# Kernel optimization log

Measured on AMD Instinct MI355X. Metric: run time of the kernel, lower is better.

## Reference

```python
import jax, jax.numpy as jnp
import numpy as np
import math

B, S, D = 4, 2048, 1024
NUM_HEADS = 16
HEAD_DIM = D // NUM_HEADS


def setup_inputs() -> dict:
    key = jax.random.key(0)
    ks = jax.random.split(key, 6)
    scale = 1.0 / math.sqrt(D)
    batch = jax.random.normal(ks[0], (B, S, D), dtype=jnp.float32)
    w_query = jax.random.normal(ks[1], (D, D), dtype=jnp.float32) * scale
    w_key = jax.random.normal(ks[2], (D, D), dtype=jnp.float32) * scale
    w_value = jax.random.normal(ks[3], (D, D), dtype=jnp.float32) * scale
    out_w = jax.random.normal(ks[4], (D, D), dtype=jnp.float32) * scale
    out_b = jax.random.normal(ks[5], (D,), dtype=jnp.float32) * 0.01
    return {"batch": batch, "w_query": w_query, "w_key": w_key,
            "w_value": w_value, "out_w": out_w, "out_b": out_b}


def reference(batch, w_query, w_key, w_value, out_w, out_b):
    b, s, _ = batch.shape
    # QKV projections (Linear with no bias): x @ W^T, here weights stored as [D,D] applied as x@W
    q = (batch @ w_query).reshape(b, s, NUM_HEADS, HEAD_DIM)
    k = (batch @ w_key).reshape(b, s, NUM_HEADS, HEAD_DIM)
    v = (batch @ w_value).reshape(b, s, NUM_HEADS, HEAD_DIM)
    # scores: [b, h, s, s]
    scores = jnp.einsum('bqhd,bkhd->bhqk', q, k)
    causal = jnp.tril(jnp.ones((s, s), dtype=bool))
    scores = jnp.where(causal, scores, -jnp.inf)
    # original divides by sqrt(head_dim) AFTER masking (-inf stays -inf)
    weights = jax.nn.softmax(scores / math.sqrt(HEAD_DIM), axis=-1)
    # dropout_percent = 0 -> identity
    out = jnp.einsum('bhqk,bkhd->bqhd', weights, v).reshape(b, s, D)
    return out @ out_w + out_b
```

## Files before the change

### kernel.cpp

```cpp
#include <hip/hip_runtime.h>
#include <hip/hip_bf16.h>

#define S_LEN 2048
#define D_DIM 1024
#define NHEAD 16
#define HDIM  64
#define BATCH 4
#define MROWS (BATCH*S_LEN)
#define QKV_LD 3072

typedef short bf16x8 __attribute__((ext_vector_type(8)));
typedef float f32x4  __attribute__((ext_vector_type(4)));
typedef float f32x16 __attribute__((ext_vector_type(16)));
typedef unsigned short u16;

#if __has_builtin(__builtin_amdgcn_exp2f)
#define EXP2(x) __builtin_amdgcn_exp2f(x)
#else
#define EXP2(x) __expf((x) * 0.6931471805599453f)
#endif

__device__ inline u16 f2bf(float f) {
  union { float f; unsigned u; } v; v.f = f;
  unsigned r = v.u + 0x7fff + ((v.u >> 16) & 1);
  return (u16)(r >> 16);
}

__device__ inline unsigned cvtpk(float lo, float hi_) {
  unsigned d;
  asm("v_cvt_pk_bf16_f32 %0, %1, %2" : "=v"(d) : "v"(lo), "v"(hi_));
  return d;
}

__device__ inline void perm32swap(unsigned& a, unsigned& b) {
  asm volatile("v_permlane32_swap_b32 %0, %1" : "+v"(a), "+v"(b));
}

__device__ inline void gload_lds16(const void* g, void* l) {
  __builtin_amdgcn_global_load_lds(
      (const __attribute__((address_space(1))) void*)g,
      (__attribute__((address_space(3))) void*)l, 16, 0, 0);
}

__global__ void cvt_x_kernel(const float* __restrict__ x, u16* __restrict__ xb, int n4) {
  int i = blockIdx.x * 256 + threadIdx.x;
  if (i >= n4) return;
  float4 v = reinterpret_cast<const float4*>(x)[i];
  ushort4 o;
  o.x = f2bf(v.x); o.y = f2bf(v.y); o.z = f2bf(v.z); o.w = f2bf(v.w);
  reinterpret_cast<ushort4*>(xb)[i] = o;
}

__global__ void transpose_w_kernel(const float* __restrict__ w, u16* __restrict__ wt) {
  __shared__ float t[32][33];
  int tx = threadIdx.x, ty = threadIdx.y;
  int n0 = blockIdx.x * 32, k0 = blockIdx.y * 32;
#pragma unroll
  for (int j = 0; j < 32; j += 8)
    t[ty + j][tx] = w[(size_t)(k0 + ty + j) * D_DIM + n0 + tx];
  __syncthreads();
#pragma unroll
  for (int j = 0; j < 32; j += 8)
    wt[(size_t)(n0 + ty + j) * D_DIM + k0 + tx] = f2bf(t[tx][ty + j]);
}

__global__ __launch_bounds__(256) void pack_k_kernel(const u16* __restrict__ QKV,
                                                     u16* __restrict__ KP) {
  int tid = threadIdx.x;
  int j = blockIdx.x, bh = blockIdx.y;
  int s = tid >> 6, lane = tid & 63;
  int lq = lane & 31, hi = lane >> 5;
  int b = bh >> 4, h = bh & 15;
  const u16* src = QKV + (size_t)(b * S_LEN + j * 32 + lq) * QKV_LD
                   + 1024 + h * HDIM + s * 16 + hi * 8;
  bf16x8 v = *(const bf16x8*)src;
  *(bf16x8*)(KP + ((size_t)(bh * 64 + j) * 4 + s) * 512 + lane * 8) = v;
}

__global__ __launch_bounds__(256) void pack_v_kernel(const u16* __restrict__ QKV,
                                                     u16* __restrict__ VP) {
  int tid = threadIdx.x;
  int j = blockIdx.x, bh = blockIdx.y;
  int c = tid >> 6, lane = tid & 63;
  int lq = lane & 31, hi = lane >> 5;
  int b = bh >> 4, h = bh & 15;
  int d = (c >> 1) * 32 + lq;
  int s0 = j * 32 + (c & 1) * 16 + hi * 8;
  const u16* src = QKV + (size_t)(b * S_LEN + s0) * QKV_LD + 2048 + h * HDIM + d;
  u16 tmp[8];
#pragma unroll
  for (int e = 0; e < 8; ++e) tmp[e] = src[(size_t)e * QKV_LD];
  *(bf16x8*)(VP + ((size_t)(bh * 64 + j) * 4 + c) * 512 + lane * 8) = *(bf16x8*)tmp;
}

#define BAR() asm volatile("s_barrier" ::: "memory")
#define WAITV(N) asm volatile("s_waitcnt vmcnt(" #N ")" ::: "memory")
#define PRIO1() __builtin_amdgcn_s_setprio(1)
#define PRIO0() __builtin_amdgcn_s_setprio(0)

#define STAGE(bufv, ab, h, gptr) {                                              \
  const u16* _s = (gptr) + (size_t)(wid * 8 + (lane >> 3)) * 1024               \
                  + (size_t)((((lane & 7) ^ (lane >> 3)) * 8));                 \
  gload_lds16(_s,              &lds[bufv][ab][(h) * 8192 + wid * 512]);         \
  gload_lds16(_s + 64 * 1024,  &lds[bufv][ab][(h) * 8192 + 4096 + wid * 512]); }

#define RDF(bufv, ab, r_, c2_) \
  (*(const bf16x8*)((const char*)&lds[bufv][ab][0] + ((r_) * 128 + ((c2_) ^ rxA))))

#define READ_ALO(bufv) { _Pragma("unroll") for (int mt = 0; mt < 4; mt++)       \
  _Pragma("unroll") for (int ks = 0; ks < 2; ks++)                              \
    fa[mt][ks] = RDF(bufv, 0, wm + mt * 16 + fr, ks * 64 + fq * 16); }
#define READ_AHI(bufv) { _Pragma("unroll") for (int mt = 0; mt < 4; mt++)       \
  _Pragma("unroll") for (int ks = 0; ks < 2; ks++)                              \
    fa[4 + mt][ks] = RDF(bufv, 0, wm + 64 + mt * 16 + fr, ks * 64 + fq * 16); }
#define READ_BLO(bufv) { _Pragma("unroll") for (int nt = 0; nt < 2; nt++)       \
  _Pragma("unroll") for (int ks = 0; ks < 2; ks++)                              \
    fb[nt][ks] = RDF(bufv, 1, wn + nt * 16 + fr, ks * 64 + fq * 16); }
#define READ_BHI(bufv) { _Pragma("unroll") for (int nt = 0; nt < 2; nt++)       \
  _Pragma("unroll") for (int ks = 0; ks < 2; ks++)                              \
    fb[2 + nt][ks] = RDF(bufv, 1, wn + 32 + nt * 16 + fr, ks * 64 + fq * 16); }

#define QUAD(mh, nh) { PRIO1();                                                 \
  _Pragma("unroll") for (int mt = 0; mt < 4; mt++)                              \
  _Pragma("unroll") for (int nt = 0; nt < 2; nt++)                              \
  _Pragma("unroll") for (int ks = 0; ks < 2; ks++)                              \
    acc[(mh) * 4 + mt][(nh) * 2 + nt] = __builtin_amdgcn_mfma_f32_16x16x32_bf16(\
        fa[(mh) * 4 + mt][ks], fb[(nh) * 2 + nt][ks],                           \
        acc[(mh) * 4 + mt][(nh) * 2 + nt], 0, 0, 0);                            \
  PRIO0(); }

#define APTR(h, kt) (A  + (size_t)(bm * 256 + (h) * 128) * 1024 + (size_t)(kt) * 64)
#define BPTR(h, kt) (Bt + (size_t)(bn * 256 + (h) * 128) * 1024 + (size_t)(kt) * 64)

template <int EPI>
__global__ __launch_bounds__(512, 2) void gemm8p_kernel(
    const u16* __restrict__ A, const u16* __restrict__ Bt,
    void* __restrict__ Cv, const float* __restrict__ bias, int nbx, int ldc) {
  __shared__ u16 lds[2][2][16384];
  const int tid = threadIdx.x, wid = tid >> 6, lane = tid & 63;
  const int fr = lane & 15, fq = lane >> 4;
  const int wm = (wid >> 2) * 128, wn = (wid & 3) * 64;
  const int rxA = (fr & 7) << 4;
  const int nwg = gridDim.x, cpx = nwg >> 3, wg = blockIdx.x;
  const int swz = (wg & 7) * cpx + (wg >> 3);
  const int bm = swz / nbx, bn = swz % nbx;

  bf16x8 fa[8][2], fb[4][2];
  f32x4 acc[8][4] = {};

  STAGE(0, 0, 0, APTR(0, 0)); STAGE(0, 0, 1, APTR(1, 0));
  STAGE(0, 1, 0, BPTR(0, 0)); STAGE(0, 1, 1, BPTR(1, 0));
  STAGE(1, 0, 0, APTR(0, 1)); STAGE(1, 0, 1, APTR(1, 1));
  WAITV(4);
  BAR();

  for (int i = 0; i < 8; i++) {
    const int t = 2 * i;
    const int t2 = (t + 2 < 16) ? t + 2 : 0;
    const int t3 = (t + 3 < 16) ? t + 3 : 0;
    READ_ALO(0); READ_BLO(0);
    STAGE(1, 1, 0, BPTR(0, t + 1));
    BAR(); QUAD(0, 0); BAR();

    READ_AHI(0);
    STAGE(1, 1, 1, BPTR(1, t + 1));
    BAR(); QUAD(1, 0); BAR();

    READ_BHI(0);
    STAGE(0, 0, 0, APTR(0, t2));
    BAR(); QUAD(0, 1); BAR();

    STAGE(0, 0, 1, APTR(1, t2));
    WAITV(4);
    BAR(); QUAD(1, 1); BAR();
    READ_ALO(1); READ_BLO(1);
    STAGE(0, 1, 0, BPTR(0, t2));
    BAR(); QUAD(0, 0); BAR();

    READ_AHI(1);
    STAGE(0, 1, 1, BPTR(1, t2));
    BAR(); QUAD(1, 0); BAR();

    READ_BHI(1);
    STAGE(1, 0, 0, APTR(0, t3));
    BAR(); QUAD(0, 1); BAR();

    STAGE(1, 0, 1, APTR(1, t3));
    WAITV(4);
    BAR(); QUAD(1, 1); BAR();
  }
  WAITV(0);

#pragma unroll
  for (int mt = 0; mt < 8; mt++)
#pragma unroll
    for (int nt = 0; nt < 4; nt++)
#pragma unroll
      for (int j = 0; j < 4; j++) {
        int row = bm * 256 + wm + mt * 16 + fq * 4 + j;
        int col = bn * 256 + wn + nt * 16 + fr;
        if (EPI == 0) {
          ((u16*)Cv)[(size_t)row * ldc + col] = f2bf(acc[mt][nt][j]);
        } else {
          ((float*)Cv)[(size_t)row * ldc + col] = acc[mt][nt][j] + bias[col];
        }
      }
}

__global__ __launch_bounds__(256) void attn_kernel(
    const u16* __restrict__ QKV, const u16* __restrict__ KP,
    const u16* __restrict__ VP, u16* __restrict__ O) {
  const int tid = threadIdx.x, wid = tid >> 6, lane = tid & 63;
  const int lq = lane & 31, hi = lane >> 5;
  int f = blockIdx.x;
  int xcd = f & 7, kk = f >> 3;
  int bh = xcd * 8 + (kk & 7);
  int qblk = 15 - (kk >> 3);
  int b = bh >> 4, h = bh & 15;
  int q0 = qblk * 128 + wid * 32;
  int q = q0 + lq;

  const u16* Qrow = QKV + (size_t)(b * S_LEN + q) * QKV_LD + h * HDIM;
  bf16x8 qf[4];
#pragma unroll
  for (int s = 0; s < 4; s++)
    qf[s] = *(const bf16x8*)(Qrow + s * 16 + hi * 8);

  const bf16x8* KPt = (const bf16x8*)KP + (size_t)bh * 64 * 4 * 64;
  const bf16x8* VPt = (const bf16x8*)VP + (size_t)bh * 64 * 4 * 64;

  f32x16 acc0 = {}, acc1 = {};
  float m = -3.0e38f, l = 0.f;
  const int nt = qblk * 4 + wid + 1;

  for (int t = 0; t < nt; ++t) {
    const int j0 = t * 32;
    const size_t fb = (size_t)t * 4 * 64 + lane;
    bf16x8 kf0 = KPt[fb], kf1 = KPt[fb + 64], kf2 = KPt[fb + 128], kf3 = KPt[fb + 192];
    bf16x8 vf00 = VPt[fb], vf01 = VPt[fb + 64], vf10 = VPt[fb + 128], vf11 = VPt[fb + 192];

    f32x16 sa = {};
    __builtin_amdgcn_s_setprio(1);
    sa = __builtin_amdgcn_mfma_f32_32x32x16_bf16(kf0, qf[0], sa, 0, 0, 0);
    sa = __builtin_amdgcn_mfma_f32_32x32x16_bf16(kf1, qf[1], sa, 0, 0, 0);
    sa = __builtin_amdgcn_mfma_f32_32x32x16_bf16(kf2, qf[2], sa, 0, 0, 0);
    sa = __builtin_amdgcn_mfma_f32_32x32x16_bf16(kf3, qf[3], sa, 0, 0, 0);
    __builtin_amdgcn_s_setprio(0);

    float p[16];
#pragma unroll
    for (int r = 0; r < 16; ++r) p[r] = sa[r] * 0.1803368801f;

    if (t == nt - 1) {
#pragma unroll
      for (int r = 0; r < 16; ++r) {
        int kidx = j0 + (r & 3) + 8 * (r >> 2) + 4 * hi;
        if (kidx > q) p[r] = -3.0e38f;
      }
    }

    float x8[8], x4[4], x2[2];
#pragma unroll
    for (int i = 0; i < 8; ++i) x8[i] = fmaxf(p[2 * i], p[2 * i + 1]);
#pragma unroll
    for (int i = 0; i < 4; ++i) x4[i] = fmaxf(x8[2 * i], x8[2 * i + 1]);
    x2[0] = fmaxf(x4[0], x4[1]); x2[1] = fmaxf(x4[2], x4[3]);
    float pm = fmaxf(x2[0], x2[1]);
    pm = fmaxf(pm, __shfl_xor(pm, 32));

    if (__any(pm > m + 11.5f)) {
      float mn = fmaxf(m, pm);
      float sc = EXP2(m - mn);
      l *= sc;
#pragma unroll
      for (int r = 0; r < 16; ++r) { acc0[r] *= sc; acc1[r] *= sc; }
      m = mn;
    }

    float rs = 0.f;
#pragma unroll
    for (int r = 0; r < 16; ++r) { p[r] = EXP2(p[r] - m); rs += p[r]; }
    rs += __shfl_xor(rs, 32);
    l += rs;

    unsigned c0 = cvtpk(p[0],  p[1]),  c1 = cvtpk(p[2],  p[3]);
    unsigned c2 = cvtpk(p[4],  p[5]),  c3 = cvtpk(p[6],  p[7]);
    unsigned c4 = cvtpk(p[8],  p[9]),  c5 = cvtpk(p[10], p[11]);
    unsigned c6 = cvtpk(p[12], p[13]), c7 = cvtpk(p[14], p[15]);
    perm32swap(c0, c2); perm32swap(c1, c3);
    perm32swap(c4, c6); perm32swap(c5, c7);
    union U4 { unsigned u[4]; bf16x8 v; } F0, F1;
    F0.u[0] = c0; F0.u[1] = c1; F0.u[2] = c2; F0.u[3] = c3;
    F1.u[0] = c4; F1.u[1] = c5; F1.u[2] = c6; F1.u[3] = c7;

    __builtin_amdgcn_s_setprio(1);
    acc0 = __builtin_amdgcn_mfma_f32_32x32x16_bf16(vf00, F0.v, acc0, 0, 0, 0);
    acc0 = __builtin_amdgcn_mfma_f32_32x32x16_bf16(vf01, F1.v, acc0, 0, 0, 0);
    acc1 = __builtin_amdgcn_mfma_f32_32x32x16_bf16(vf10, F0.v, acc1, 0, 0, 0);
    acc1 = __builtin_amdgcn_mfma_f32_32x32x16_bf16(vf11, F1.v, acc1, 0, 0, 0);
    __builtin_amdgcn_s_setprio(0);
  }

  float inv = 1.f / l;
  u16* Orow = O + (size_t)(b * S_LEN + q) * D_DIM + h * HDIM;
#pragma unroll
  for (int g = 0; g < 4; ++g) {
    ushort4 o4;
    o4.x = f2bf(acc0[g * 4 + 0] * inv);
    o4.y = f2bf(acc0[g * 4 + 1] * inv);
    o4.z = f2bf(acc0[g * 4 + 2] * inv);
    o4.w = f2bf(acc0[g * 4 + 3] * inv);
    *(ushort4*)(Orow + 8 * g + 4 * hi) = o4;
  }
#pragma unroll
  for (int g = 0; g < 4; ++g) {
    ushort4 o4;
    o4.x = f2bf(acc1[g * 4 + 0] * inv);
    o4.y = f2bf(acc1[g * 4 + 1] * inv);
    o4.z = f2bf(acc1[g * 4 + 2] * inv);
    o4.w = f2bf(acc1[g * 4 + 3] * inv);
    *(ushort4*)(Orow + 32 + 8 * g + 4 * hi) = o4;
  }
}

extern "C" void kernel_launch(void* const* d_in, const int* in_sizes, int n_in,
                              void* d_out, int out_size, void* d_ws, size_t ws_size,
                              hipStream_t stream) {
  const float* x  = (const float*)d_in[0];
  const float* wq = (const float*)d_in[1];
  const float* wk = (const float*)d_in[2];
  const float* wv = (const float*)d_in[3];
  const float* wo = (const float*)d_in[4];
  const float* ob = (const float*)d_in[5];
  float* out = (float*)d_out;

  char* ws = (char*)d_ws;
  u16* Xb    = (u16*)(ws);
  u16* Ab    = (u16*)(ws);
  u16* QKV   = (u16*)(ws + (size_t)16 * 1024 * 1024);
  u16* KPb   = (u16*)(ws + (size_t)64 * 1024 * 1024);
  u16* VPb   = (u16*)(ws + (size_t)80 * 1024 * 1024);
  u16* WqkvT = (u16*)(ws + (size_t)96 * 1024 * 1024);
  u16* WoT   = (u16*)(ws + (size_t)102 * 1024 * 1024);

  cvt_x_kernel<<<(MROWS * D_DIM / 4) / 256, 256, 0, stream>>>(x, Xb, MROWS * D_DIM / 4);

  dim3 tb(32, 8);
  transpose_w_kernel<<<dim3(32, 32), tb, 0, stream>>>(wq, WqkvT);
  transpose_w_kernel<<<dim3(32, 32), tb, 0, stream>>>(wk, WqkvT + 1024 * 1024);
  transpose_w_kernel<<<dim3(32, 32), tb, 0, stream>>>(wv, WqkvT + 2 * 1024 * 1024);
  transpose_w_kernel<<<dim3(32, 32), tb, 0, stream>>>(wo, WoT);

  gemm8p_kernel<0><<<dim3((MROWS / 256) * (QKV_LD / 256)), 512, 0, stream>>>(
      Xb, WqkvT, QKV, nullptr, QKV_LD / 256, QKV_LD);

  pack_k_kernel<<<dim3(64, 64), 256, 0, stream>>>(QKV, KPb);
  pack_v_kernel<<<dim3(64, 64), 256, 0, stream>>>(QKV, VPb);

  attn_kernel<<<dim3(1024), 256, 0, stream>>>(QKV, KPb, VPb, Ab);

  gemm8p_kernel<1><<<dim3((MROWS / 256) * (D_DIM / 256)), 512, 0, stream>>>(
      Ab, WoT, out, ob, D_DIM / 256, D_DIM);
}
```

Before: 196.4 us.

## Shrink GEMM tile to 256x128 with 4x2 wave layout for more workgroups

Changes the GEMM workgroup tile from 256x256 to 256x128. The 8 waves now form a 4x2 grid, each computing 64x64 instead of 128x64, and the grids double to fill more CUs. That matters most for the out-projection GEMM, which previously launched only 128 workgroups. LDS staging is rewritten into separate A and B arrays with per-64-row units, and the launch_bounds occupancy hint is dropped. The cost is lower arithmetic intensity per tile and twice the A-operand reloads.

```diff
diff --git a/kernel.cpp b/kernel.cpp
--- a/kernel.cpp
+++ b/kernel.cpp
@@ -98,59 +98,61 @@
 #define PRIO1() __builtin_amdgcn_s_setprio(1)
 #define PRIO0() __builtin_amdgcn_s_setprio(0)
 
-#define STAGE(bufv, ab, h, gptr) {                                              \
-  const u16* _s = (gptr) + (size_t)(wid * 8 + (lane >> 3)) * 1024               \
-                  + (size_t)((((lane & 7) ^ (lane >> 3)) * 8));                 \
-  gload_lds16(_s,              &lds[bufv][ab][(h) * 8192 + wid * 512]);         \
-  gload_lds16(_s + 64 * 1024,  &lds[bufv][ab][(h) * 8192 + 4096 + wid * 512]); }
-
-#define RDF(bufv, ab, r_, c2_) \
-  (*(const bf16x8*)((const char*)&lds[bufv][ab][0] + ((r_) * 128 + ((c2_) ^ rxA))))
-
-#define READ_ALO(bufv) { _Pragma("unroll") for (int mt = 0; mt < 4; mt++)       \
-  _Pragma("unroll") for (int ks = 0; ks < 2; ks++)                              \
-    fa[mt][ks] = RDF(bufv, 0, wm + mt * 16 + fr, ks * 64 + fq * 16); }
-#define READ_AHI(bufv) { _Pragma("unroll") for (int mt = 0; mt < 4; mt++)       \
-  _Pragma("unroll") for (int ks = 0; ks < 2; ks++)                              \
-    fa[4 + mt][ks] = RDF(bufv, 0, wm + 64 + mt * 16 + fr, ks * 64 + fq * 16); }
-#define READ_BLO(bufv) { _Pragma("unroll") for (int nt = 0; nt < 2; nt++)       \
-  _Pragma("unroll") for (int ks = 0; ks < 2; ks++)                              \
-    fb[nt][ks] = RDF(bufv, 1, wn + nt * 16 + fr, ks * 64 + fq * 16); }
-#define READ_BHI(bufv) { _Pragma("unroll") for (int nt = 0; nt < 2; nt++)       \
-  _Pragma("unroll") for (int ks = 0; ks < 2; ks++)                              \
-    fb[2 + nt][ks] = RDF(bufv, 1, wn + 32 + nt * 16 + fr, ks * 64 + fq * 16); }
+#define STAGE_U(ldsArr, u, gptr) {                                              \
+  const u16* _s = (gptr) + (size_t)((u) * 64 + (tid >> 3)) * 1024               \
+                  + (size_t)(((tid & 7) ^ ((tid >> 3) & 7)) * 8);               \
+  gload_lds16(_s, &ldsArr[((u) * 64 + wid * 8) * 64]); }
+
+#define RDF(ldsArr, r_, c2_) \
+  (*(const bf16x8*)((const char*)&ldsArr[0] + ((r_) * 128 + ((c2_) ^ rxA))))
+
+#define READ_A_LO(buf) { _Pragma("unroll") for (int mt = 0; mt < 2; mt++)       \
+  _Pragma("unroll") for (int ks = 0; ks < 2; ks++)                              \
+    fa[mt][ks] = RDF(lA[buf], wm + mt * 16 + fr, ks * 64 + fq * 16); }
+#define READ_A_HI(buf) { _Pragma("unroll") for (int mt = 0; mt < 2; mt++)       \
+  _Pragma("unroll") for (int ks = 0; ks < 2; ks++)                              \
+    fa[2 + mt][ks] = RDF(lA[buf], wm + 32 + mt * 16 + fr, ks * 64 + fq * 16); }
+#define READ_B_LO(buf) { _Pragma("unroll") for (int nt = 0; nt < 2; nt++)       \
+  _Pragma("unroll") for (int ks = 0; ks < 2; ks++)                              \
+    fb[nt][ks] = RDF(lB[buf], wn + nt * 16 + fr, ks * 64 + fq * 16); }
+#define READ_B_HI(buf) { _Pragma("unroll") for (int nt = 0; nt < 2; nt++)       \
+  _Pragma("unroll") for (int ks = 0; ks < 2; ks++)                              \
+    fb[2 + nt][ks] = RDF(lB[buf], wn + 32 + nt * 16 + fr, ks * 64 + fq * 16); }
 
 #define QUAD(mh, nh) { PRIO1();                                                 \
-  _Pragma("unroll") for (int mt = 0; mt < 4; mt++)                              \
+  _Pragma("unroll") for (int mt = 0; mt < 2; mt++)                              \
   _Pragma("unroll") for (int nt = 0; nt < 2; nt++)                              \
   _Pragma("unroll") for (int ks = 0; ks < 2; ks++)                              \
-    acc[(mh) * 4 + mt][(nh) * 2 + nt] = __builtin_amdgcn_mfma_f32_16x16x32_bf16(\
-        fa[(mh) * 4 + mt][ks], fb[(nh) * 2 + nt][ks],                           \
-        acc[(mh) * 4 + mt][(nh) * 2 + nt], 0, 0, 0);                            \
+    acc[(mh) * 2 + mt][(nh) * 2 + nt] = __builtin_amdgcn_mfma_f32_16x16x32_bf16(\
+        fa[(mh) * 2 + mt][ks], fb[(nh) * 2 + nt][ks],                           \
+        acc[(mh) * 2 + mt][(nh) * 2 + nt], 0, 0, 0);                            \
   PRIO0(); }
 
-#define APTR(h, kt) (A  + (size_t)(bm * 256 + (h) * 128) * 1024 + (size_t)(kt) * 64)
-#define BPTR(h, kt) (Bt + (size_t)(bn * 256 + (h) * 128) * 1024 + (size_t)(kt) * 64)
+#define APTR(kt) (A  + (size_t)(bm * 256) * 1024 + (size_t)(kt) * 64)
+#define BPTR(kt) (Bt + (size_t)(bn * 128) * 1024 + (size_t)(kt) * 64)
 
 template <int EPI>
-__global__ __launch_bounds__(512, 2) void gemm8p_kernel(
+__global__ __launch_bounds__(512) void gemm8p_kernel(
     const u16* __restrict__ A, const u16* __restrict__ Bt,
     void* __restrict__ Cv, const float* __restrict__ bias, int nbx, int ldc) {
-  __shared__ u16 lds[2][2][16384];
+  __shared__ u16 lA[2][16384];
+  __shared__ u16 lB[2][8192];
   const int tid = threadIdx.x, wid = tid >> 6, lane = tid & 63;
   const int fr = lane & 15, fq = lane >> 4;
-  const int wm = (wid >> 2) * 128, wn = (wid & 3) * 64;
+  const int wm = (wid >> 1) * 64, wn = (wid & 1) * 64;
   const int rxA = (fr & 7) << 4;
   const int nwg = gridDim.x, cpx = nwg >> 3, wg = blockIdx.x;
   const int swz = (wg & 7) * cpx + (wg >> 3);
   const int bm = swz / nbx, bn = swz % nbx;
 
-  bf16x8 fa[8][2], fb[4][2];
-  f32x4 acc[8][4] = {};
-
-  STAGE(0, 0, 0, APTR(0, 0)); STAGE(0, 0, 1, APTR(1, 0));
-  STAGE(0, 1, 0, BPTR(0, 0)); STAGE(0, 1, 1, BPTR(1, 0));
-  STAGE(1, 0, 0, APTR(0, 1)); STAGE(1, 0, 1, APTR(1, 1));
+  bf16x8 fa[4][2], fb[4][2];
+  f32x4 acc[4][4] = {};
+
+  STAGE_U(lA[0], 0, APTR(0)); STAGE_U(lA[0], 1, APTR(0));
+  STAGE_U(lA[0], 2, APTR(0)); STAGE_U(lA[0], 3, APTR(0));
+  STAGE_U(lB[0], 0, BPTR(0)); STAGE_U(lB[0], 1, BPTR(0));
+  STAGE_U(lA[1], 0, APTR(1)); STAGE_U(lA[1], 1, APTR(1));
+  STAGE_U(lA[1], 2, APTR(1)); STAGE_U(lA[1], 3, APTR(1));
   WAITV(4);
   BAR();
 
@@ -158,47 +160,47 @@
     const int t = 2 * i;
     const int t2 = (t + 2 < 16) ? t + 2 : 0;
     const int t3 = (t + 3 < 16) ? t + 3 : 0;
-    READ_ALO(0); READ_BLO(0);
-    STAGE(1, 1, 0, BPTR(0, t + 1));
+    READ_A_LO(0); READ_B_LO(0);
+    STAGE_U(lB[1], 0, BPTR(t + 1));
     BAR(); QUAD(0, 0); BAR();
 
-    READ_AHI(0);
-    STAGE(1, 1, 1, BPTR(1, t + 1));
+    READ_A_HI(0);
+    STAGE_U(lB[1], 1, BPTR(t + 1));
     BAR(); QUAD(1, 0); BAR();
 
-    READ_BHI(0);
-    STAGE(0, 0, 0, APTR(0, t2));
+    READ_B_HI(0);
+    STAGE_U(lA[0], 0, APTR(t2)); STAGE_U(lA[0], 1, APTR(t2));
     BAR(); QUAD(0, 1); BAR();
 
-    STAGE(0, 0, 1, APTR(1, t2));
+    STAGE_U(lA[0], 2, APTR(t2)); STAGE_U(lA[0], 3, APTR(t2));
     WAITV(4);
     BAR(); QUAD(1, 1); BAR();
-    READ_ALO(1); READ_BLO(1);
-    STAGE(0, 1, 0, BPTR(0, t2));
+    READ_A_LO(1); READ_B_LO(1);
+    STAGE_U(lB[0], 0, BPTR(t2));
     BAR(); QUAD(0, 0); BAR();
 
-    READ_AHI(1);
-    STAGE(0, 1, 1, BPTR(1, t2));
+    READ_A_HI(1);
+    STAGE_U(lB[0], 1, BPTR(t2));
     BAR(); QUAD(1, 0); BAR();
 
-    READ_BHI(1);
-    STAGE(1, 0, 0, APTR(0, t3));
+    READ_B_HI(1);
+    STAGE_U(lA[1], 0, APTR(t3)); STAGE_U(lA[1], 1, APTR(t3));
     BAR(); QUAD(0, 1); BAR();
 
-    STAGE(1, 0, 1, APTR(1, t3));
+    STAGE_U(lA[1], 2, APTR(t3)); STAGE_U(lA[1], 3, APTR(t3));
     WAITV(4);
     BAR(); QUAD(1, 1); BAR();
   }
   WAITV(0);
 
 #pragma unroll
-  for (int mt = 0; mt < 8; mt++)
+  for (int mt = 0; mt < 4; mt++)
 #pragma unroll
     for (int nt = 0; nt < 4; nt++)
 #pragma unroll
       for (int j = 0; j < 4; j++) {
         int row = bm * 256 + wm + mt * 16 + fq * 4 + j;
-        int col = bn * 256 + wn + nt * 16 + fr;
+        int col = bn * 128 + wn + nt * 16 + fr;
         if (EPI == 0) {
           ((u16*)Cv)[(size_t)row * ldc + col] = f2bf(acc[mt][nt][j]);
         } else {
@@ -351,14 +353,14 @@
   transpose_w_kernel<<<dim3(32, 32), tb, 0, stream>>>(wv, WqkvT + 2 * 1024 * 1024);
   transpose_w_kernel<<<dim3(32, 32), tb, 0, stream>>>(wo, WoT);
 
-  gemm8p_kernel<0><<<dim3((MROWS / 256) * (QKV_LD / 256)), 512, 0, stream>>>(
-      Xb, WqkvT, QKV, nullptr, QKV_LD / 256, QKV_LD);
+  gemm8p_kernel<0><<<dim3((MROWS / 256) * (QKV_LD / 128)), 512, 0, stream>>>(
+      Xb, WqkvT, QKV, nullptr, QKV_LD / 128, QKV_LD);
 
   pack_k_kernel<<<dim3(64, 64), 256, 0, stream>>>(QKV, KPb);
   pack_v_kernel<<<dim3(64, 64), 256, 0, stream>>>(QKV, VPb);
 
   attn_kernel<<<dim3(1024), 256, 0, stream>>>(QKV, KPb, VPb, Ab);
 
-  gemm8p_kernel<1><<<dim3((MROWS / 256) * (D_DIM / 256)), 512, 0, stream>>>(
-      Ab, WoT, out, ob, D_DIM / 256, D_DIM);
-}
+  gemm8p_kernel<1><<<dim3((MROWS / 256) * (D_DIM / 128)), 512, 0, stream>>>(
+      Ab, WoT, out, ob, D_DIM / 128, D_DIM);
+}
```

Result: faster. 191.7 us (-2.4%).
